# Performance work log

Hardware: AMD Instinct MI355X
Metric: run time of the kernel (lower is better)

## Reference

```python
import jax, jax.numpy as jnp
import numpy as np

B, NLB, NPB, SDIM = 128, 32, 160, 256  # complexes, ligand atoms, pocket CAs, scalar dim


def _uniform(key, shape, fan_in):
    # kaiming_uniform_(a=sqrt(5)) -> U(-1/sqrt(fan_in), 1/sqrt(fan_in))
    bound = 1.0 / np.sqrt(fan_in)
    return jax.random.uniform(key, shape, jnp.float32, -bound, bound)


def setup_inputs() -> dict:
    key = jax.random.key(0)
    k1, k2, k3, k4, k5 = jax.random.split(key, 5)
    NL, NP = B * NLB, B * NPB
    # block-diagonal cross adjacency: every ligand atom paired with every pocket CA
    # of the same complex (same as (batch_ligand[:,None]==batch_pocket[None,:]).nonzero().T)
    l = np.repeat(np.arange(NL, dtype=np.int32), NPB)
    p = (np.arange(B, dtype=np.int32)[:, None, None] * NPB
         + np.zeros((1, NLB, 1), dtype=np.int32)
         + np.arange(NPB, dtype=np.int32)[None, None, :]).reshape(-1)
    return {
        "s_ligand": jax.random.normal(k1, (NL, SDIM), jnp.float32),
        "s_pocket": jax.random.normal(k2, (NP, SDIM), jnp.float32),
        "l": jnp.asarray(l),
        "p": jnp.asarray(p),
        "W1": _uniform(k3, (SDIM // 2, SDIM), SDIM),
        "b1": jnp.zeros((SDIM // 2,), jnp.float32),
        "W2": _uniform(k4, (SDIM // 4, SDIM // 2), SDIM // 2),
        "b2": jnp.zeros((SDIM // 4,), jnp.float32),
        "W3": _uniform(k5, (1, SDIM // 4), SDIM // 4),
        "b3": jnp.zeros((1,), jnp.float32),
    }


def reference(s_ligand, s_pocket, l, p, W1, b1, W2, b2, W3, b3):
    # gather cross-pair embeddings and sum: s[e] = s_ligand[l[e]] + s_pocket[p[e]]
    s = s_ligand[l] + s_pocket[p]                      # [E, sdim]
    h = jax.nn.silu(s @ W1.T + b1)                     # [E, sdim/2]
    h = jax.nn.silu(h @ W2.T + b2)                     # [E, sdim/4]
    out = jax.nn.relu(h @ W3.T + b3)                   # [E, 1]
    return out.squeeze(-1)                             # [E]
```

## Files before the change

### kernel.cpp

```cpp
#include <hip/hip_runtime.h>
#include <hip/hip_bf16.h>


#define B_CPLX   128
#define NLB      32
#define NPB      160
#define SDIM     256
#define H1DIM    128
#define NL_TOT   (B_CPLX * NLB)
#define NP_TOT   (B_CPLX * NPB)
#define NROWS    (NL_TOT + NP_TOT)
#define E_TOT    (B_CPLX * NLB * NPB)

#define W1_LDS_STRIDE 264
#define JT_CHUNK 16
#define ZP_STRIDE 132

#define EDGE_BLOCKS (B_CPLX * 10)

#define NEG_LOG2E -1.4426950408889634f
#define NEG_LN2   -0.69314718055994531f

typedef __bf16 bf16x8 __attribute__((ext_vector_type(8)));
typedef __bf16 bf16x2 __attribute__((ext_vector_type(2)));
typedef unsigned short ushortx8 __attribute__((ext_vector_type(8)));
typedef unsigned short ushortx4 __attribute__((ext_vector_type(4)));
typedef unsigned uintx4 __attribute__((ext_vector_type(4)));
typedef unsigned uintx2 __attribute__((ext_vector_type(2)));
typedef float f32x4 __attribute__((ext_vector_type(4)));
typedef float f32x2 __attribute__((ext_vector_type(2)));

#if __has_builtin(__builtin_amdgcn_exp2f)
#define EXP2F(x) __builtin_amdgcn_exp2f(x)
#else
#define EXP2F(x) exp2f(x)
#endif

__device__ __forceinline__ unsigned perm_hi16u(unsigned u0, unsigned u1) {
    return __builtin_amdgcn_perm(u1, u0, 0x07060302u);
}

__device__ __forceinline__ unsigned cvt2_rne(float x0, float x1) {
    f32x2 p = {x0, x1};
    bf16x2 b = __builtin_convertvector(p, bf16x2);
    return __builtin_bit_cast(unsigned, b);
}

__device__ __forceinline__ uintx2 pack4_rne_u(f32x4 v) {
    uintx2 r;
    r[0] = cvt2_rne(v[0], v[1]);
    r[1] = cvt2_rne(v[2], v[3]);
    return r;
}

__device__ __forceinline__ bf16x8 pack8_rne(const float* x) {
    uintx4 h;
#pragma unroll
    for (int j = 0; j < 4; ++j) h[j] = cvt2_rne(x[2 * j], x[2 * j + 1]);
    return __builtin_bit_cast(bf16x8, h);
}

__device__ __forceinline__ void pack_split(const float* x, bf16x8& hi, bf16x8& lo) {
    uintx4 h, l;
#pragma unroll
    for (int j = 0; j < 4; ++j) {
        float x0 = x[2 * j], x1 = x[2 * j + 1];
        unsigned u0 = __builtin_bit_cast(unsigned, x0);
        unsigned u1 = __builtin_bit_cast(unsigned, x1);
        h[j] = perm_hi16u(u0, u1);
        float hf0 = __builtin_bit_cast(float, u0 & 0xFFFF0000u);
        float hf1 = __builtin_bit_cast(float, u1 & 0xFFFF0000u);
        l[j] = cvt2_rne(x0 - hf0, x1 - hf1);
    }
    hi = __builtin_bit_cast(bf16x8, h);
    lo = __builtin_bit_cast(bf16x8, l);
}

__device__ __forceinline__ float silu_u(float t) {
    float e = EXP2F(t);
    float r = __builtin_amdgcn_rcpf(1.0f + e);
    return t * r;
}

__global__ __launch_bounds__(256) void proj_kernel(
    const float* __restrict__ s_lig, const float* __restrict__ s_poc,
    const float* __restrict__ W1,    const float* __restrict__ b1,
    const float* __restrict__ W2,
    float* __restrict__ Z,           unsigned short* __restrict__ W2F)
{
    __shared__ unsigned short w1s[64 * W1_LDS_STRIDE];

    const int tid  = threadIdx.x;
    const int tg   = blockIdx.x >> 1;
    const int half = blockIdx.x & 1;

    if (blockIdx.x == 0) {
#pragma unroll
        for (int s = 0; s < 4; ++s) {
            const int slot   = tid + s * 256;
            const int lane_s = slot & 63;
            const int chunk  = slot >> 6;
            const int nt     = chunk >> 2;
            const int ks     = chunk & 3;
            const int n      = nt * 16 + (lane_s & 15);
            const int k0     = ks * 32 + (lane_s >> 4) * 8;
            const float* wsrc = W2 + (size_t)n * H1DIM + k0;
            f32x4 wa = *(const f32x4*)wsrc;
            f32x4 wb = *(const f32x4*)(wsrc + 4);
            uintx4 us;
            us[0] = cvt2_rne(wa[0], wa[1]);
            us[1] = cvt2_rne(wa[2], wa[3]);
            us[2] = cvt2_rne(wb[0], wb[1]);
            us[3] = cvt2_rne(wb[2], wb[3]);
            *(uintx4*)(&W2F[slot * 8]) = us;
        }
    }

    {
        const f32x4* w4 = (const f32x4*)(W1 + (size_t)half * 64 * SDIM);
#pragma unroll
        for (int r = 0; r < 2; ++r) {
            f32x4 t[8];
#pragma unroll
            for (int s = 0; s < 8; ++s) t[s] = w4[tid + (r * 8 + s) * 256];
#pragma unroll
            for (int s = 0; s < 8; ++s) {
                const int u = tid + (r * 8 + s) * 256;
                const int n = u >> 6;
                const int k4 = u & 63;
                uintx2 us = pack4_rne_u(t[s] * NEG_LOG2E);
                *(uintx2*)(&w1s[n * W1_LDS_STRIDE + k4 * 4]) = us;
            }
        }
    }
    __syncthreads();

    const int lane = tid & 63;
    const int widx = tid >> 6;
    const int c    = lane & 15;
    const int q    = lane >> 4;
    const int tile = tg * 4 + widx;
    const int row  = tile * 16 + c;

    const float* src = (row < NL_TOT) ? (s_lig + (size_t)row * SDIM)
                                      : (s_poc + (size_t)(row - NL_TOT) * SDIM);

    f32x4 acc[4];
#pragma unroll
    for (int nt = 0; nt < 4; ++nt) acc[nt] = (f32x4){0.f, 0.f, 0.f, 0.f};

#pragma unroll
    for (int ks = 0; ks < 8; ++ks) {
        const int k0 = ks * 32 + q * 8;
        f32x4 xa = *reinterpret_cast<const f32x4*>(src + k0);
        f32x4 xb = *reinterpret_cast<const f32x4*>(src + k0 + 4);
        float xv[8] = {xa[0], xa[1], xa[2], xa[3], xb[0], xb[1], xb[2], xb[3]};
        bf16x8 ahi, alo;
        pack_split(xv, ahi, alo);
        bf16x8 bfrag[4];
#pragma unroll
        for (int nt = 0; nt < 4; ++nt)
            bfrag[nt] = *reinterpret_cast<const bf16x8*>(
                &w1s[(nt * 16 + c) * W1_LDS_STRIDE + k0]);
#pragma unroll
        for (int nt = 0; nt < 4; ++nt)
            acc[nt] = __builtin_amdgcn_mfma_f32_16x16x32_bf16(ahi, bfrag[nt], acc[nt], 0, 0, 0);
#pragma unroll
        for (int nt = 0; nt < 4; ++nt)
            acc[nt] = __builtin_amdgcn_mfma_f32_16x16x32_bf16(alo, bfrag[nt], acc[nt], 0, 0, 0);
    }

    const int mb = tile * 16 + q * 4;
#pragma unroll
    for (int nt = 0; nt < 4; ++nt) {
        const int n = half * 64 + nt * 16 + c;
        const float bias = b1[n] * NEG_LOG2E;
#pragma unroll
        for (int r = 0; r < 4; ++r) {
            const int m = mb + r;
            float v = acc[nt][r];
            if (m < NL_TOT) v += bias;
            Z[(size_t)m * H1DIM + n] = v;
        }
    }
}

__global__ __launch_bounds__(512) void edge_kernel(
    const float* __restrict__ Z,  const unsigned short* __restrict__ W2F,
    const float* __restrict__ b2, const float* __restrict__ W3,
    const float* __restrict__ b3, float* __restrict__ out)
{
    __shared__ float zp[JT_CHUNK * ZP_STRIDE];
    __shared__ float zl[NLB * H1DIM];
    __shared__ unsigned short w2s[16 * 64 * 8];

    const int tid = threadIdx.x;
    const int b   = blockIdx.x / 10;
    const int jt  = blockIdx.x - b * 10;

    {
#pragma unroll
        for (int s = 0; s < 2; ++s) {
            const int slot = tid + s * 512;
            *(ushortx8*)(&w2s[slot * 8]) = *(const ushortx8*)(&W2F[slot * 8]);
        }
    }

    {
        const float* zpg = Z + (size_t)(NL_TOT + b * NPB + jt * JT_CHUNK) * H1DIM;
        const int row = tid >> 5;
        const int c4  = tid & 31;
        *(f32x4*)(&zp[row * ZP_STRIDE + c4 * 4]) =
            *(const f32x4*)(zpg + (size_t)row * H1DIM + c4 * 4);
    }

    {
        const float* zlg = Z + (size_t)(b * NLB) * H1DIM;
#pragma unroll
        for (int s = 0; s < 2; ++s) {
            const int u   = tid + s * 512;
            const int row = u >> 5;
            const int c4  = u & 31;
            *(f32x4*)(&zl[row * H1DIM + c4 * 4]) =
                *(const f32x4*)(zlg + (size_t)row * H1DIM + c4 * 4);
        }
    }

    const int lane = tid & 63;
    const int widx = tid >> 6;
    const int c    = lane & 15;
    const int q    = lane >> 4;

    f32x4 b2v[4], w3v[4];
#pragma unroll
    for (int nt = 0; nt < 4; ++nt) {
        f32x4 bv = *(const f32x4*)(b2 + nt * 16 + q * 4);
        f32x4 wv = *(const f32x4*)(W3 + nt * 16 + q * 4);
        b2v[nt] = bv * NEG_LOG2E;
        w3v[nt] = wv * NEG_LN2;
    }
    const float b3v = b3[0];

    __syncthreads();

    const float* prow = &zp[c * ZP_STRIDE];
    const unsigned short* wbase = &w2s[lane * 8];

    f32x4 acc[4][4];
#pragma unroll
    for (int a = 0; a < 4; ++a)
#pragma unroll
        for (int nt = 0; nt < 4; ++nt) acc[a][nt] = b2v[nt];

    const float* lrow0 = &zl[(widx * 4) * H1DIM];

#pragma unroll
    for (int ks = 0; ks < 4; ++ks) {
        const int k0 = ks * 32 + q * 8;
        bf16x8 bfr[4];
#pragma unroll
        for (int nt = 0; nt < 4; ++nt)
            bfr[nt] = *(const bf16x8*)(wbase + (nt * 4 + ks) * 512);
        f32x4 pa = *(const f32x4*)(prow + k0);
        f32x4 pb = *(const f32x4*)(prow + k0 + 4);
#pragma unroll
        for (int a = 0; a < 4; ++a) {
            f32x4 la0 = *(const f32x4*)(lrow0 + a * H1DIM + k0);
            f32x4 la1 = *(const f32x4*)(lrow0 + a * H1DIM + k0 + 4);
            float hv[8];
#pragma unroll
            for (int j = 0; j < 4; ++j) {
                hv[j]     = silu_u(pa[j] + la0[j]);
                hv[4 + j] = silu_u(pb[j] + la1[j]);
            }
            bf16x8 af = pack8_rne(hv);
#pragma unroll
            for (int nt = 0; nt < 4; ++nt)
                acc[a][nt] = __builtin_amdgcn_mfma_f32_16x16x32_bf16(bfr[nt], af, acc[a][nt], 0, 0, 0);
        }
    }

#pragma unroll
    for (int at = 0; at < 4; ++at) {
        const f32x4* A = acc[at];
        float s0 = 0.f, s1 = 0.f, s2 = 0.f, s3 = 0.f;
#pragma unroll
        for (int nt = 0; nt < 4; ++nt) {
            s0 += silu_u(A[nt][0]) * w3v[nt][0];
            s1 += silu_u(A[nt][1]) * w3v[nt][1];
            s2 += silu_u(A[nt][2]) * w3v[nt][2];
            s3 += silu_u(A[nt][3]) * w3v[nt][3];
        }
        float v = (s0 + s1) + (s2 + s3);
        v += __shfl_xor(v, 16);
        v += __shfl_xor(v, 32);
        if (lane < 16) {
            const int e0 = (b * NLB + widx * 4 + at) * NPB + jt * JT_CHUNK;
            out[e0 + lane] = fmaxf(v + b3v, 0.0f);
        }
    }
}

extern "C" void kernel_launch(void* const* d_in, const int* in_sizes, int n_in,
                              void* d_out, int out_size, void* d_ws, size_t ws_size,
                              hipStream_t stream)
{
    const float* s_lig = (const float*)d_in[0];
    const float* s_poc = (const float*)d_in[1];
    const float* W1    = (const float*)d_in[4];
    const float* b1    = (const float*)d_in[5];
    const float* W2    = (const float*)d_in[6];
    const float* b2    = (const float*)d_in[7];
    const float* W3    = (const float*)d_in[8];
    const float* b3    = (const float*)d_in[9];

    float* Z = (float*)d_ws;
    unsigned short* W2F = (unsigned short*)(Z + (size_t)NROWS * H1DIM);

    hipLaunchKernelGGL(proj_kernel, dim3(NROWS / 16 / 4 * 2), dim3(256), 0, stream,
                       s_lig, s_poc, W1, b1, W2, Z, W2F);
    hipLaunchKernelGGL(edge_kernel, dim3(EDGE_BLOCKS), dim3(512), 0, stream,
                       Z, W2F, b2, W3, b3, (float*)d_out);
}
```

Measured before the change: 126.4 us.

## Fuse pocket projection into edge kernel and shrink projection kernel to ligand rows

Pocket rows are no longer projected through W1 in the first kernel and round-tripped through the Z workspace. Instead each edge block computes its 16 pocket rows' W1 projection directly with MFMA, using a W1 fragment array pre-packed to bf16 by extra blocks of the first kernel. This removes the global write and read of pocket Z and shrinks the projection grid. The cost is extra per-block compute and s_poc reads in the edge kernel; each pocket tile is projected once per block, so there is no redundant recomputation.

```diff
diff --git a/kernel.cpp b/kernel.cpp
--- a/kernel.cpp
+++ b/kernel.cpp
@@ -18,13 +18,16 @@
 
 #define EDGE_BLOCKS (B_CPLX * 10)
 
+#define LIG_BLOCKS  128
+#define W1F_BLOCKS  4
+#define PROJ_BLOCKS (LIG_BLOCKS + W1F_BLOCKS + 1)
+
 #define NEG_LOG2E -1.4426950408889634f
 #define NEG_LN2   -0.69314718055994531f
 
 typedef __bf16 bf16x8 __attribute__((ext_vector_type(8)));
 typedef __bf16 bf16x2 __attribute__((ext_vector_type(2)));
 typedef unsigned short ushortx8 __attribute__((ext_vector_type(8)));
-typedef unsigned short ushortx4 __attribute__((ext_vector_type(4)));
 typedef unsigned uintx4 __attribute__((ext_vector_type(4)));
 typedef unsigned uintx2 __attribute__((ext_vector_type(2)));
 typedef float f32x4 __attribute__((ext_vector_type(4)));
@@ -83,38 +86,64 @@
 }
 
 __global__ __launch_bounds__(256) void proj_kernel(
-    const float* __restrict__ s_lig, const float* __restrict__ s_poc,
-    const float* __restrict__ W1,    const float* __restrict__ b1,
-    const float* __restrict__ W2,
-    float* __restrict__ Z,           unsigned short* __restrict__ W2F)
+    const float* __restrict__ s_lig, const float* __restrict__ W1,
+    const float* __restrict__ b1,    const float* __restrict__ W2,
+    float* __restrict__ Z,           unsigned short* __restrict__ W2F,
+    unsigned short* __restrict__ W1F)
 {
+    const int bid = blockIdx.x;
+    const int tid = threadIdx.x;
+
+    if (bid >= LIG_BLOCKS) {
+        const int u = bid - LIG_BLOCKS;
+        if (u < W1F_BLOCKS) {
+#pragma unroll
+            for (int s = 0; s < 4; ++s) {
+                const int slot   = u * 1024 + tid + s * 256;
+                const int lane_s = slot & 63;
+                const int chunk  = slot >> 6;
+                const int nblk   = chunk >> 3;
+                const int ks     = chunk & 7;
+                const int n      = nblk * 16 + (lane_s & 15);
+                const int k0     = ks * 32 + (lane_s >> 4) * 8;
+                const float* wsrc = W1 + (size_t)n * SDIM + k0;
+                f32x4 wa = *(const f32x4*)wsrc * NEG_LOG2E;
+                f32x4 wb = *(const f32x4*)(wsrc + 4) * NEG_LOG2E;
+                uintx4 us;
+                us[0] = cvt2_rne(wa[0], wa[1]);
+                us[1] = cvt2_rne(wa[2], wa[3]);
+                us[2] = cvt2_rne(wb[0], wb[1]);
+                us[3] = cvt2_rne(wb[2], wb[3]);
+                *(uintx4*)(&W1F[slot * 8]) = us;
+            }
+        } else {
+#pragma unroll
+            for (int s = 0; s < 4; ++s) {
+                const int slot   = tid + s * 256;
+                const int lane_s = slot & 63;
+                const int chunk  = slot >> 6;
+                const int nt     = chunk >> 2;
+                const int ks     = chunk & 3;
+                const int n      = nt * 16 + (lane_s & 15);
+                const int k0     = ks * 32 + (lane_s >> 4) * 8;
+                const float* wsrc = W2 + (size_t)n * H1DIM + k0;
+                f32x4 wa = *(const f32x4*)wsrc;
+                f32x4 wb = *(const f32x4*)(wsrc + 4);
+                uintx4 us;
+                us[0] = cvt2_rne(wa[0], wa[1]);
+                us[1] = cvt2_rne(wa[2], wa[3]);
+                us[2] = cvt2_rne(wb[0], wb[1]);
+                us[3] = cvt2_rne(wb[2], wb[3]);
+                *(uintx4*)(&W2F[slot * 8]) = us;
+            }
+        }
+        return;
+    }
+
     __shared__ unsigned short w1s[64 * W1_LDS_STRIDE];
 
-    const int tid  = threadIdx.x;
-    const int tg   = blockIdx.x >> 1;
-    const int half = blockIdx.x & 1;
-
-    if (blockIdx.x == 0) {
-#pragma unroll
-        for (int s = 0; s < 4; ++s) {
-            const int slot   = tid + s * 256;
-            const int lane_s = slot & 63;
-            const int chunk  = slot >> 6;
-            const int nt     = chunk >> 2;
-            const int ks     = chunk & 3;
-            const int n      = nt * 16 + (lane_s & 15);
-            const int k0     = ks * 32 + (lane_s >> 4) * 8;
-            const float* wsrc = W2 + (size_t)n * H1DIM + k0;
-            f32x4 wa = *(const f32x4*)wsrc;
-            f32x4 wb = *(const f32x4*)(wsrc + 4);
-            uintx4 us;
-            us[0] = cvt2_rne(wa[0], wa[1]);
-            us[1] = cvt2_rne(wa[2], wa[3]);
-            us[2] = cvt2_rne(wb[0], wb[1]);
-            us[3] = cvt2_rne(wb[2], wb[3]);
-            *(uintx4*)(&W2F[slot * 8]) = us;
-        }
-    }
+    const int tg   = bid >> 1;
+    const int half = bid & 1;
 
     {
         const f32x4* w4 = (const f32x4*)(W1 + (size_t)half * 64 * SDIM);
@@ -142,8 +171,7 @@
     const int tile = tg * 4 + widx;
     const int row  = tile * 16 + c;
 
-    const float* src = (row < NL_TOT) ? (s_lig + (size_t)row * SDIM)
-                                      : (s_poc + (size_t)(row - NL_TOT) * SDIM);
+    const float* src = s_lig + (size_t)row * SDIM;
 
     f32x4 acc[4];
 #pragma unroll
@@ -176,17 +204,15 @@
         const int n = half * 64 + nt * 16 + c;
         const float bias = b1[n] * NEG_LOG2E;
 #pragma unroll
-        for (int r = 0; r < 4; ++r) {
-            const int m = mb + r;
-            float v = acc[nt][r];
-            if (m < NL_TOT) v += bias;
-            Z[(size_t)m * H1DIM + n] = v;
-        }
+        for (int r = 0; r < 4; ++r)
+            Z[(size_t)(mb + r) * H1DIM + n] = acc[nt][r] + bias;
     }
 }
 
 __global__ __launch_bounds__(512) void edge_kernel(
     const float* __restrict__ Z,  const unsigned short* __restrict__ W2F,
+    const unsigned short* __restrict__ W1F,
+    const float* __restrict__ s_poc,
     const float* __restrict__ b2, const float* __restrict__ W3,
     const float* __restrict__ b3, float* __restrict__ out)
 {
@@ -198,20 +224,17 @@
     const int b   = blockIdx.x / 10;
     const int jt  = blockIdx.x - b * 10;
 
+    const int lane = tid & 63;
+    const int widx = tid >> 6;
+    const int c    = lane & 15;
+    const int q    = lane >> 4;
+
     {
 #pragma unroll
         for (int s = 0; s < 2; ++s) {
             const int slot = tid + s * 512;
             *(ushortx8*)(&w2s[slot * 8]) = *(const ushortx8*)(&W2F[slot * 8]);
         }
-    }
-
-    {
-        const float* zpg = Z + (size_t)(NL_TOT + b * NPB + jt * JT_CHUNK) * H1DIM;
-        const int row = tid >> 5;
-        const int c4  = tid & 31;
-        *(f32x4*)(&zp[row * ZP_STRIDE + c4 * 4]) =
-            *(const f32x4*)(zpg + (size_t)row * H1DIM + c4 * 4);
     }
 
     {
@@ -226,10 +249,26 @@
         }
     }
 
-    const int lane = tid & 63;
-    const int widx = tid >> 6;
-    const int c    = lane & 15;
-    const int q    = lane >> 4;
+    {
+        const float* sp = s_poc + (size_t)(b * NPB + jt * JT_CHUNK + c) * SDIM;
+        const unsigned short* wf = W1F + ((size_t)widx * 8 * 64 + lane) * 8;
+        f32x4 pacc = (f32x4){0.f, 0.f, 0.f, 0.f};
+#pragma unroll 2
+        for (int ks = 0; ks < 8; ++ks) {
+            const int k0 = ks * 32 + q * 8;
+            f32x4 xa = *(const f32x4*)(sp + k0);
+            f32x4 xb = *(const f32x4*)(sp + k0 + 4);
+            float xv[8] = {xa[0], xa[1], xa[2], xa[3], xb[0], xb[1], xb[2], xb[3]};
+            bf16x8 phi, plo;
+            pack_split(xv, phi, plo);
+            bf16x8 bfr = *(const bf16x8*)(wf + (size_t)ks * 64 * 8);
+            pacc = __builtin_amdgcn_mfma_f32_16x16x32_bf16(phi, bfr, pacc, 0, 0, 0);
+            pacc = __builtin_amdgcn_mfma_f32_16x16x32_bf16(plo, bfr, pacc, 0, 0, 0);
+        }
+#pragma unroll
+        for (int r = 0; r < 4; ++r)
+            zp[(q * 4 + r) * ZP_STRIDE + widx * 16 + c] = pacc[r];
+    }
 
     f32x4 b2v[4], w3v[4];
 #pragma unroll
@@ -316,9 +355,10 @@
 
     float* Z = (float*)d_ws;
     unsigned short* W2F = (unsigned short*)(Z + (size_t)NROWS * H1DIM);
-
-    hipLaunchKernelGGL(proj_kernel, dim3(NROWS / 16 / 4 * 2), dim3(256), 0, stream,
-                       s_lig, s_poc, W1, b1, W2, Z, W2F);
+    unsigned short* W1F = W2F + 1024 * 8;
+
+    hipLaunchKernelGGL(proj_kernel, dim3(PROJ_BLOCKS), dim3(256), 0, stream,
+                       s_lig, W1, b1, W2, Z, W2F, W1F);
     hipLaunchKernelGGL(edge_kernel, dim3(EDGE_BLOCKS), dim3(512), 0, stream,
-                       Z, W2F, b2, W3, b3, (float*)d_out);
-}
+                       Z, W2F, W1F, s_poc, b2, W3, b3, (float*)d_out);
+}
```

Measured after the change: 132.1 us. +4.5%, slower.
